# Optimization experiments

Hardware: AMD Instinct MI355X
Metric: run time of the kernel (lower is better)

Reference implementation:

```python
import jax, jax.numpy as jnp
import numpy as np

B, S, H = 1, 4096, 2048
NH, NKV, HD = 16, 4, 128  # query heads, kv heads, head_dim
THETA = 1000000.0
NEG = -1e9


def setup_inputs() -> dict:
    key = jax.random.key(0)
    ks = jax.random.split(key, 5)
    hidden_states = jax.random.normal(ks[0], (B, S, H), jnp.float32) * 0.02
    Wq = jax.random.normal(ks[1], (H, NH * HD), jnp.float32) * 0.02
    Wk = jax.random.normal(ks[2], (H, NKV * HD), jnp.float32) * 0.02
    Wv = jax.random.normal(ks[3], (H, NKV * HD), jnp.float32) * 0.02
    Wo = jax.random.normal(ks[4], (H, H), jnp.float32) * 0.02
    # additive causal mask [B,1,S,S]
    causal = jnp.tril(jnp.ones((S, S), bool))
    attention_mask = jnp.where(causal, 0.0, NEG).astype(jnp.float32)[None, None]
    position_ids = jnp.arange(S, dtype=jnp.int32)[None]
    return dict(hidden_states=hidden_states, Wq=Wq, Wk=Wk, Wv=Wv, Wo=Wo,
                attention_mask=attention_mask, position_ids=position_ids)


def _rotate_half(x):
    return jnp.concatenate([-x[..., HD // 2:], x[..., :HD // 2]], axis=-1)


def reference(hidden_states, Wq, Wk, Wv, Wo, attention_mask, position_ids):
    # projections -> [B, heads, S, HD]
    q = (hidden_states @ Wq).reshape(B, S, NH, HD).transpose(0, 2, 1, 3)
    k = (hidden_states @ Wk).reshape(B, S, NKV, HD).transpose(0, 2, 1, 3)
    v = (hidden_states @ Wv).reshape(B, S, NKV, HD).transpose(0, 2, 1, 3)

    # RoPE (HF style: freqs duplicated across halves, rotate_half)
    inv_freq = 1.0 / (THETA ** (jnp.arange(0, HD, 2, dtype=jnp.float32) / HD))
    freqs = position_ids.astype(jnp.float32)[..., None] * inv_freq  # [B,S,HD/2]
    emb = jnp.concatenate([freqs, freqs], axis=-1)                  # [B,S,HD]
    cos = jnp.cos(emb)[:, None].astype(q.dtype)                     # [B,1,S,HD]
    sin = jnp.sin(emb)[:, None].astype(q.dtype)
    q = q * cos + _rotate_half(q) * sin
    k = k * cos + _rotate_half(k) * sin

    # GQA: repeat each kv head consecutively (matches torch repeat_kv)
    rep = NH // NKV
    k = jnp.repeat(k, rep, axis=1)
    v = jnp.repeat(v, rep, axis=1)

    scale = 1.0 / jnp.sqrt(jnp.float32(HD))
    scores = jnp.einsum('bhqd,bhkd->bhqk', q, k) * scale + attention_mask
    attn = jax.nn.softmax(scores.astype(jnp.float32), axis=-1).astype(q.dtype)
    out = jnp.einsum('bhqk,bhkd->bhqd', attn, v)  # [B,NH,S,HD]
    out = out.transpose(0, 2, 1, 3).reshape(B, S, H)
    return out @ Wo
```

## Files before the change

### kernel.cpp

```cpp
#include <hip/hip_runtime.h>
#include <stdint.h>

typedef uint16_t u16;
typedef __bf16  bf16x8 __attribute__((ext_vector_type(8)));
typedef float   f32x4  __attribute__((ext_vector_type(4)));
typedef float   f32x16 __attribute__((ext_vector_type(16)));
typedef uint16_t u16x8 __attribute__((ext_vector_type(8), may_alias));
typedef uint32_t u32x4 __attribute__((ext_vector_type(4)));

typedef const __attribute__((address_space(1))) void* gas_p;
typedef __attribute__((address_space(3))) void* las_p;

#define SCALE2 0.1275430214486847f

__device__ __forceinline__ void load_lds16(const void* g, void* l) {
    __builtin_amdgcn_global_load_lds((gas_p)g, (las_p)l, 16, 0, 0);
}

__device__ __forceinline__ u16 f2bf(float f) {
    uint32_t u = __builtin_bit_cast(uint32_t, f);
    u += 0x7FFFu + ((u >> 16) & 1u);
    return (u16)(u >> 16);
}
__device__ __forceinline__ float bf2f(u16 h) {
    uint32_t u = ((uint32_t)h) << 16;
    return __builtin_bit_cast(float, u);
}
__device__ __forceinline__ bf16x8 ld_frag(const u16* p) {
    u16x8 t = *(const u16x8*)p;
    return __builtin_bit_cast(bf16x8, t);
}
__device__ __forceinline__ uint32_t cvt_pk_bf16(float lo, float hi) {
    uint32_t r;
    asm("v_cvt_pk_bf16_f32 %0, %1, %2" : "=v"(r) : "v"(lo), "v"(hi));
    return r;
}
__device__ __forceinline__ void plane32_swap(uint32_t& a, uint32_t& b) {
    asm("v_permlane32_swap_b32 %0, %1" : "+v"(a), "+v"(b));
}

__global__ __launch_bounds__(256) void convert_hidden(const float* __restrict__ in,
                                                      u16* __restrict__ out, int n8) {
    int i = blockIdx.x * 256 + threadIdx.x;
    if (i >= n8) return;
    const float* p = in + (size_t)i * 8;
    u16x8 o;
#pragma unroll
    for (int j = 0; j < 8; j++) o[j] = f2bf(p[j]);
    *(u16x8*)(out + (size_t)i * 8) = o;
}

__global__ __launch_bounds__(256) void transpose_cvt(const float* __restrict__ in,
                                                     u16* __restrict__ out,
                                                     int R, int C) {
    __shared__ u16 tile[64][65];
    const int tx = threadIdx.x;
    const int bc = blockIdx.x * 64;
    const int br = blockIdx.y * 64;
#pragma unroll
    for (int i = 0; i < 16; i++) {
        int idx = tx + i * 256;
        int r = idx >> 6, c = idx & 63;
        tile[r][c] = f2bf(in[(size_t)(br + r) * C + bc + c]);
    }
    __syncthreads();
#pragma unroll
    for (int i = 0; i < 16; i++) {
        int idx = tx + i * 256;
        int r = idx >> 6, c = idx & 63;
        out[(size_t)(bc + r) * R + br + c] = tile[c][r];
    }
}

__global__ __launch_bounds__(256) void transpose_b16(const u16* __restrict__ in,
                                                     u16* __restrict__ out,
                                                     int R, int C, int ldin, int off) {
    __shared__ u16 tile[64][65];
    const int tx = threadIdx.x;
    const int bc = blockIdx.x * 64;
    const int br = blockIdx.y * 64;
#pragma unroll
    for (int i = 0; i < 16; i++) {
        int idx = tx + i * 256;
        int r = idx >> 6, c = idx & 63;
        tile[r][c] = in[(size_t)(br + r) * ldin + off + bc + c];
    }
    __syncthreads();
#pragma unroll
    for (int i = 0; i < 16; i++) {
        int idx = tx + i * 256;
        int r = idx >> 6, c = idx & 63;
        out[(size_t)(bc + r) * R + br + c] = tile[c][r];
    }
}

#define TM 128
#define TN 128
#define TK 32

__global__ __launch_bounds__(256) void gemm_qkv(const u16* __restrict__ A,
                                                const u16* __restrict__ WqT,
                                                const u16* __restrict__ WkvT,
                                                u16* __restrict__ Qb,
                                                u16* __restrict__ KVb) {
    __shared__ u16 As[TM * TK];
    __shared__ u16 Bs[TN * TK];
    const int K = 2048;
    const int tid  = threadIdx.x;
    const int wave = tid >> 6;
    const int lane = tid & 63;
    const int l15  = lane & 15;
    const int quad = lane >> 4;
    const int m0 = blockIdx.y * TM;
    const int n0 = blockIdx.x * TN;
    const u16* Bt;
    u16* C;
    int ldC, cbase;
    if (n0 < 2048) { Bt = WqT + (size_t)n0 * K;          C = Qb;  ldC = 2048; cbase = n0; }
    else           { Bt = WkvT + (size_t)(n0 - 2048) * K; C = KVb; ldC = 1024; cbase = n0 - 2048; }
    const int wm = (wave >> 1) * 64;
    const int wn = (wave & 1) * 64;

    f32x4 acc[4][4] = {};

    const int srow = tid >> 2;
    const int scol = (tid & 3) * 8;
    const u16* Ap0 = A  + (size_t)(m0 + srow) * K + scol;
    const u16* Ap1 = A  + (size_t)(m0 + 64 + srow) * K + scol;
    const u16* Bp0 = Bt + (size_t)srow * K + scol;
    const u16* Bp1 = Bt + (size_t)(64 + srow) * K + scol;
    u16* AsD0 = As + wave * 512;
    u16* AsD1 = As + 2048 + wave * 512;
    u16* BsD0 = Bs + wave * 512;
    u16* BsD1 = Bs + 2048 + wave * 512;

    for (int k0 = 0; k0 < K; k0 += TK) {
        load_lds16(Ap0 + k0, AsD0);
        load_lds16(Ap1 + k0, AsD1);
        load_lds16(Bp0 + k0, BsD0);
        load_lds16(Bp1 + k0, BsD1);
        __syncthreads();
        bf16x8 af[4], bfr[4];
#pragma unroll
        for (int i = 0; i < 4; i++)
            af[i] = ld_frag(&As[(wm + i * 16 + l15) * TK + quad * 8]);
#pragma unroll
        for (int j = 0; j < 4; j++)
            bfr[j] = ld_frag(&Bs[(wn + j * 16 + l15) * TK + quad * 8]);
#pragma unroll
        for (int i = 0; i < 4; i++)
#pragma unroll
            for (int j = 0; j < 4; j++)
                acc[i][j] = __builtin_amdgcn_mfma_f32_16x16x32_bf16(af[i], bfr[j], acc[i][j], 0, 0, 0);
        __syncthreads();
    }
#pragma unroll
    for (int i = 0; i < 4; i++)
#pragma unroll
        for (int j = 0; j < 4; j++)
#pragma unroll
            for (int r = 0; r < 4; r++) {
                int row = m0 + wm + i * 16 + quad * 4 + r;
                int col = cbase + wn + j * 16 + l15;
                C[(size_t)row * ldC + col] = f2bf(acc[i][j][r]);
            }
}

template <bool F32OUT>
__global__ __launch_bounds__(256) void gemm_bt(const u16* __restrict__ A,
                                               const u16* __restrict__ Bt,
                                               void* __restrict__ Cp,
                                               int M, int N, int K) {
    __shared__ u16 As[TM * TK];
    __shared__ u16 Bs[TN * TK];
    const int tid  = threadIdx.x;
    const int wave = tid >> 6;
    const int lane = tid & 63;
    const int l15  = lane & 15;
    const int quad = lane >> 4;
    const int m0 = blockIdx.y * TM;
    const int n0 = blockIdx.x * TN;
    const int wm = (wave >> 1) * 64;
    const int wn = (wave & 1) * 64;

    f32x4 acc[4][4] = {};

    const int srow = tid >> 2;
    const int scol = (tid & 3) * 8;
    const u16* Ap0 = A  + (size_t)(m0 + srow) * K + scol;
    const u16* Ap1 = A  + (size_t)(m0 + 64 + srow) * K + scol;
    const u16* Bp0 = Bt + (size_t)(n0 + srow) * K + scol;
    const u16* Bp1 = Bt + (size_t)(n0 + 64 + srow) * K + scol;
    u16* AsD0 = As + wave * 512;
    u16* AsD1 = As + 2048 + wave * 512;
    u16* BsD0 = Bs + wave * 512;
    u16* BsD1 = Bs + 2048 + wave * 512;

    for (int k0 = 0; k0 < K; k0 += TK) {
        load_lds16(Ap0 + k0, AsD0);
        load_lds16(Ap1 + k0, AsD1);
        load_lds16(Bp0 + k0, BsD0);
        load_lds16(Bp1 + k0, BsD1);
        __syncthreads();
        bf16x8 af[4], bfr[4];
#pragma unroll
        for (int i = 0; i < 4; i++)
            af[i] = ld_frag(&As[(wm + i * 16 + l15) * TK + quad * 8]);
#pragma unroll
        for (int j = 0; j < 4; j++)
            bfr[j] = ld_frag(&Bs[(wn + j * 16 + l15) * TK + quad * 8]);
#pragma unroll
        for (int i = 0; i < 4; i++)
#pragma unroll
            for (int j = 0; j < 4; j++)
                acc[i][j] = __builtin_amdgcn_mfma_f32_16x16x32_bf16(af[i], bfr[j], acc[i][j], 0, 0, 0);
        __syncthreads();
    }
#pragma unroll
    for (int i = 0; i < 4; i++)
#pragma unroll
        for (int j = 0; j < 4; j++)
#pragma unroll
            for (int r = 0; r < 4; r++) {
                int row = m0 + wm + i * 16 + quad * 4 + r;
                int col = n0 + wn + j * 16 + l15;
                if (F32OUT)
                    ((float*)Cp)[(size_t)row * N + col] = acc[i][j][r];
                else
                    ((u16*)Cp)[(size_t)row * N + col] = f2bf(acc[i][j][r]);
            }
}

__global__ __launch_bounds__(256) void rope_kernel(u16* __restrict__ Q,
                                                   u16* __restrict__ KV) {
    int g = blockIdx.x * 256 + threadIdx.x;
    int d = g & 63;
    int row = g >> 6;
    int s = row / 20;
    int hh = row - s * 20;
    u16* buf = (hh < 16) ? (Q + (size_t)s * 2048 + hh * 128)
                         : (KV + (size_t)s * 1024 + (hh - 16) * 128);
    float p = (float)s;
    float angle = p * exp2f((float)d * (-19.931568569324174f / 64.0f));
    float sc = (hh < 16) ? SCALE2 : 1.0f;
    float c = cosf(angle) * sc, sn = sinf(angle) * sc;
    float x0 = bf2f(buf[d]), x1 = bf2f(buf[d + 64]);
    buf[d]      = f2bf(x0 * c - x1 * sn);
    buf[d + 64] = f2bf(x1 * c + x0 * sn);
}

#define QK1(CC, MSK)                                                           \
  do {                                                                         \
    const int krow_ = (CC) * 32 + l31;                                         \
    f32x16 sv_ = {};                                                           \
    _Pragma("unroll")                                                          \
    for (int dk = 0; dk < 8; dk++) {                                           \
      bf16x8 kf = ld_frag(&Kb[krow_ * 128 + (((dk * 2 + hi8) + krow_) & 15) * 8]); \
      sv_ = __builtin_amdgcn_mfma_f32_32x32x16_bf16(kf, qf[dk], sv_, 0, 0, 0); \
    }                                                                          \
    float p_[16]; float rs_ = 0.f;                                             \
    const int kvbs_ = kv0 + (CC) * 32 + 4 * hi8;                               \
    _Pragma("unroll")                                                          \
    for (int r = 0; r < 16; r++) {                                             \
      float pe = exp2f(sv_[r]);                                                \
      if (MSK) { int kvv = kvbs_ + (r & 3) + 8 * (r >> 2);                     \
                 pe = (kvv <= qrow) ? pe : 0.f; }                              \
      p_[r] = pe; rs_ += pe;                                                   \
    }                                                                          \
    lr += rs_;                                                                 \
    uint32_t w0 = cvt_pk_bf16(p_[0], p_[1]);                                   \
    uint32_t w1 = cvt_pk_bf16(p_[2], p_[3]);                                   \
    uint32_t w2 = cvt_pk_bf16(p_[4], p_[5]);                                   \
    uint32_t w3 = cvt_pk_bf16(p_[6], p_[7]);                                   \
    plane32_swap(w0, w2); plane32_swap(w1, w3);                                \
    uint32_t w4 = cvt_pk_bf16(p_[8], p_[9]);                                   \
    uint32_t w5 = cvt_pk_bf16(p_[10], p_[11]);                                 \
    uint32_t w6 = cvt_pk_bf16(p_[12], p_[13]);                                 \
    plane32_swap(w4, w6);                                                      \
    uint32_t w7 = cvt_pk_bf16(p_[14], p_[15]);                                 \
    plane32_swap(w5, w7);                                                      \
    u32x4 a0_ = {w0, w1, w2, w3}, a1_ = {w4, w5, w6, w7};                      \
    bf16x8 pa0_ = __builtin_bit_cast(bf16x8, a0_);                             \
    bf16x8 pa1_ = __builtin_bit_cast(bf16x8, a1_);                             \
    _Pragma("unroll")                                                          \
    for (int ks2 = 0; ks2 < 2; ks2++) {                                        \
      bf16x8 pa_ = ks2 ? pa1_ : pa0_;                                          \
      _Pragma("unroll")                                                        \
      for (int nt = 0; nt < 4; nt++) {                                         \
        const int d_ = nt * 32 + l31;                                          \
        bf16x8 vf = ld_frag(&Vb[d_ * 64 + ((((CC) * 4 + ks2 * 2 + hi8) + d_) & 7) * 8]); \
        acc[nt] = __builtin_amdgcn_mfma_f32_32x32x16_bf16(pa_, vf, acc[nt], 0, 0, 0); \
      }                                                                        \
    }                                                                          \
  } while (0)

__global__ __launch_bounds__(256, 2) void flash_attn9(const u16* __restrict__ Q,
                                                      const u16* __restrict__ KVb,
                                                      const u16* __restrict__ VT,
                                                      u16* __restrict__ Op0,
                                                      u16* __restrict__ Op1,
                                                      float* __restrict__ Lp) {
    __shared__ u16 Ks[2][8192];
    __shared__ u16 Vs[2][8192];
    const int tid  = threadIdx.x;
    const int ww   = tid >> 6;
    const int lane = tid & 63;
    const int l31  = lane & 31;
    const int hi8  = lane >> 5;
    const int bid  = blockIdx.x;
    const int h    = (bid & 7) * 2 + ((bid >> 3) & 1);
    const int rest = bid >> 4;
    const int j    = 31 - (rest >> 1);
    const int s    = rest & 1;
    const int kvh  = h >> 2;
    const int qg0  = j * 128 + ww * 32;
    const int qrow = qg0 + l31;
    const int dW   = qg0 >> 6;
    const int kb0  = s * (j + 1);
    const int kb1  = kb0 + (j + 1);

    bf16x8 qf[8];
    {
        const u16* qp = Q + (size_t)qrow * 2048 + h * 128 + hi8 * 8;
#pragma unroll
        for (int dk = 0; dk < 8; dk++) qf[dk] = ld_frag(qp + dk * 16);
    }

    const u16* srcK[4];
    const u16* srcV[4];
#pragma unroll
    for (int r = 0; r < 4; r++) {
        int p = r * 256 + tid;
        int kv = p >> 4;
        srcK[r] = KVb + (size_t)kv * 1024 + kvh * 128 + ((((p & 15) - kv) & 15) * 8);
        int d = p >> 3;
        srcV[r] = VT + (size_t)(kvh * 128 + d) * 4096 + ((((p & 7) - (d & 7)) & 7) * 8);
    }

    f32x16 acc[4] = {};
    float lr = 0.f;

#pragma unroll
    for (int r = 0; r < 4; r++) {
        load_lds16(srcK[r] + (size_t)(kb0 * 64) * 1024, &Ks[0][r * 2048 + ww * 512]);
        load_lds16(srcV[r] + kb0 * 64, &Vs[0][r * 2048 + ww * 512]);
    }
    asm volatile("s_waitcnt vmcnt(0)" ::: "memory");
    __syncthreads();

    for (int kvb = kb0; kvb < kb1; kvb++) {
        const int cur = (kvb - kb0) & 1;
        if (kvb + 1 < kb1) {
            const int kvn = (kvb + 1) * 64;
#pragma unroll
            for (int r = 0; r < 4; r++) {
                load_lds16(srcK[r] + (size_t)kvn * 1024, &Ks[cur ^ 1][r * 2048 + ww * 512]);
                load_lds16(srcV[r] + kvn, &Vs[cur ^ 1][r * 2048 + ww * 512]);
            }
        }
        const u16* Kb = Ks[cur];
        const u16* Vb = Vs[cur];
        const int kv0 = kvb * 64;

        if (kvb < dW) {
            QK1(0, 0);
            QK1(1, 0);
        } else if (kvb == dW) {
            QK1(0, 1);
            QK1(1, 1);
        }

        asm volatile("s_waitcnt vmcnt(0)" ::: "memory");
        __syncthreads();
    }

    float lt = lr + __shfl_xor(lr, 32);
    if (lane < 32) Lp[(s * 16 + h) * 4096 + qg0 + l31] = lt;
    u16* Ops = s ? Op1 : Op0;
#pragma unroll
    for (int r = 0; r < 16; r++) {
        int qr = (r & 3) + 8 * (r >> 2) + 4 * hi8;
        u16* op = Ops + (size_t)(qg0 + qr) * 2048 + h * 128 + l31;
#pragma unroll
        for (int nt = 0; nt < 4; nt++)
            op[nt * 32] = f2bf(acc[nt][r]);
    }
}

__global__ __launch_bounds__(256) void merge_o(u16* __restrict__ o0,
                                               const u16* __restrict__ o1,
                                               const float* __restrict__ Lp) {
    int i = blockIdx.x * 256 + threadIdx.x;
    size_t base = (size_t)i * 8;
    int row = (int)(base >> 11);
    int h   = (int)((base >> 7) & 15);
    float inv = 1.0f / (Lp[h * 4096 + row] + Lp[(16 + h) * 4096 + row]);
    u16x8 a = *(const u16x8*)(o0 + base);
    u16x8 b = *(const u16x8*)(o1 + base);
    u16x8 o;
#pragma unroll
    for (int jj = 0; jj < 8; jj++)
        o[jj] = f2bf((bf2f(a[jj]) + bf2f(b[jj])) * inv);
    *(u16x8*)(o0 + base) = o;
}

__global__ __launch_bounds__(256, 2) void flash_attn7(const u16* __restrict__ Q,
                                                      const u16* __restrict__ KVb,
                                                      const u16* __restrict__ VT,
                                                      u16* __restrict__ O) {
    __shared__ u16 Ks[2][8192];
    __shared__ u16 Vs[2][8192];
    __shared__ float Llds[4][32];
    const int tid  = threadIdx.x;
    const int ww   = tid >> 6;
    const int lane = tid & 63;
    const int l31  = lane & 31;
    const int hi8  = lane >> 5;
    const int bid  = blockIdx.x;
    const int h    = bid >> 5;
    const int cls  = bid & 31;
    const int bx   = cls >> 1;
    const int z    = cls & 1;
    const int kvh  = h >> 2;
    const int qt0  = z ? (3968 - bx * 128) : (bx * 128);
    const int qg0  = qt0 + ww * 32;
    const int qrow = qg0 + l31;
    const int dW   = qg0 >> 6;
    const int nkv  = (qt0 >> 6) + 2;

    bf16x8 qf[8];
    {
        const u16* qp = Q + (size_t)qrow * 2048 + h * 128 + hi8 * 8;
#pragma unroll
        for (int dk = 0; dk < 8; dk++) qf[dk] = ld_frag(qp + dk * 16);
    }

    const u16* srcK[4];
    const u16* srcV[4];
#pragma unroll
    for (int r = 0; r < 4; r++) {
        int p = r * 256 + tid;
        int kv = p >> 4;
        srcK[r] = KVb + (size_t)kv * 1024 + kvh * 128 + ((((p & 15) - kv) & 15) * 8);
        int d = p >> 3;
        srcV[r] = VT + (size_t)(kvh * 128 + d) * 4096 + ((((p & 7) - (d & 7)) & 7) * 8);
    }

    f32x16 acc[4] = {};
    float lr = 0.f;

#pragma unroll
    for (int r = 0; r < 4; r++) {
        load_lds16(srcK[r], &Ks[0][r * 2048 + ww * 512]);
        load_lds16(srcV[r], &Vs[0][r * 2048 + ww * 512]);
    }
    asm volatile("s_waitcnt vmcnt(0)" ::: "memory");
    __syncthreads();

    for (int kvb = 0; kvb < nkv; kvb++) {
        const int cur = kvb & 1;
        if (kvb + 1 < nkv) {
            const int kvn = (kvb + 1) * 64;
#pragma unroll
            for (int r = 0; r < 4; r++) {
                load_lds16(srcK[r] + (size_t)kvn * 1024, &Ks[cur ^ 1][r * 2048 + ww * 512]);
                load_lds16(srcV[r] + kvn, &Vs[cur ^ 1][r * 2048 + ww * 512]);
            }
        }
        const u16* Kb = Ks[cur];
        const u16* Vb = Vs[cur];
        const int kv0 = kvb * 64;

        if (kvb < dW) {
            QK1(0, 0);
            QK1(1, 0);
        } else if (kvb == dW) {
            QK1(0, 1);
            QK1(1, 1);
        }

        asm volatile("s_waitcnt vmcnt(0)" ::: "memory");
        __syncthreads();
    }

    float lt = lr + __shfl_xor(lr, 32);
    if (lane < 32) Llds[ww][l31] = lt;
    __syncthreads();
#pragma unroll
    for (int r = 0; r < 16; r++) {
        int qr = (r & 3) + 8 * (r >> 2) + 4 * hi8;
        float linv = 1.0f / Llds[ww][qr];
        u16* op = O + (size_t)(qg0 + qr) * 2048 + h * 128 + l31;
#pragma unroll
        for (int nt = 0; nt < 4; nt++)
            op[nt * 32] = f2bf(acc[nt][r] * linv);
    }
}

extern "C" void kernel_launch(void* const* d_in, const int* in_sizes, int n_in,
                              void* d_out, int out_size, void* d_ws, size_t ws_size,
                              hipStream_t stream) {
    const float* hidden = (const float*)d_in[0];
    const float* Wq = (const float*)d_in[1];
    const float* Wk = (const float*)d_in[2];
    const float* Wv = (const float*)d_in[3];
    const float* Wo = (const float*)d_in[4];
    float* out = (float*)d_out;

    u16* ws   = (u16*)d_ws;
    u16* Hb   = ws;
    u16* Qb   = Hb   + 8388608;
    u16* KVb  = Qb   + 8388608;
    u16* WqT  = KVb  + 4194304;
    u16* WkvT = WqT  + 4194304;
    u16* VT   = WkvT + 2097152;
    u16* Op1  = VT   + 4194304;
    const size_t WS_SPLIT = (size_t)(31457280 + 8388608) * 2;

    convert_hidden<<<4096, 256, 0, stream>>>(hidden, Hb, 1048576);

    transpose_cvt<<<dim3(32, 32), 256, 0, stream>>>(Wq, WqT, 2048, 2048);
    transpose_cvt<<<dim3(8, 32), 256, 0, stream>>>(Wk, WkvT, 2048, 512);
    transpose_cvt<<<dim3(8, 32), 256, 0, stream>>>(Wv, WkvT + 1048576, 2048, 512);

    gemm_qkv<<<dim3(24, 32), 256, 0, stream>>>(Hb, WqT, WkvT, Qb, KVb);

    u16* WoT = WqT;
    transpose_cvt<<<dim3(32, 32), 256, 0, stream>>>(Wo, WoT, 2048, 2048);

    rope_kernel<<<dim3(20480), 256, 0, stream>>>(Qb, KVb);

    transpose_b16<<<dim3(8, 64), 256, 0, stream>>>(KVb, VT, 4096, 512, 1024, 512);

    u16* Ob = Hb;
    if (ws_size >= WS_SPLIT) {
        float* Lp = (float*)WkvT;
        flash_attn9<<<dim3(1024), 256, 0, stream>>>(Qb, KVb, VT, Ob, Op1, Lp);
        merge_o<<<dim3(4096), 256, 0, stream>>>(Ob, Op1, Lp);
    } else {
        flash_attn7<<<dim3(512), 256, 0, stream>>>(Qb, KVb, VT, Ob);
    }

    gemm_bt<true><<<dim3(16, 32), 256, 0, stream>>>(Ob, WoT, out, 4096, 2048, 2048);
}
```

Measured before the change: 388.0 us.

## Split K and V prefetch around QK and PV phases in flash attention

The attention loop now issues the next tile's K loads first and computes QK^T and softmax probabilities for both 32-column chunks into registers. Only then does it issue the next V loads, and it runs the PV MFMAs after a barrier, using partial vmcnt waits so the V prefetch can stay in flight while the current tile is processed. The V tile in LDS also gets a new swizzled layout that packs two d-rows per 128-element row. The gain depends on the hardware memory counters retiring in issue order, and holding the P fragments across the barrier raises register pressure.

```diff
diff --git a/kernel.cpp b/kernel.cpp
--- a/kernel.cpp
+++ b/kernel.cpp
@@ -248,6 +248,57 @@
     buf[d]      = f2bf(x0 * c - x1 * sn);
     buf[d + 64] = f2bf(x1 * c + x0 * sn);
 }
+
+#define QKSM(CC, MSK, PA)                                                      \
+  do {                                                                         \
+    const int krow_ = (CC) * 32 + l31;                                         \
+    f32x16 sv_ = {};                                                           \
+    _Pragma("unroll")                                                          \
+    for (int dk = 0; dk < 8; dk++) {                                           \
+      bf16x8 kf = ld_frag(&Kb[krow_ * 128 + (((dk * 2 + hi8) + krow_) & 15) * 8]); \
+      sv_ = __builtin_amdgcn_mfma_f32_32x32x16_bf16(kf, qf[dk], sv_, 0, 0, 0); \
+    }                                                                          \
+    float p_[16]; float rs_ = 0.f;                                             \
+    const int kvbs_ = kv0 + (CC) * 32 + 4 * hi8;                               \
+    _Pragma("unroll")                                                          \
+    for (int r = 0; r < 16; r++) {                                             \
+      float pe = exp2f(sv_[r]);                                                \
+      if (MSK) { int kvv = kvbs_ + (r & 3) + 8 * (r >> 2);                     \
+                 pe = (kvv <= qrow) ? pe : 0.f; }                              \
+      p_[r] = pe; rs_ += pe;                                                   \
+    }                                                                          \
+    lr += rs_;                                                                 \
+    uint32_t w0 = cvt_pk_bf16(p_[0], p_[1]);                                   \
+    uint32_t w1 = cvt_pk_bf16(p_[2], p_[3]);                                   \
+    uint32_t w2 = cvt_pk_bf16(p_[4], p_[5]);                                   \
+    uint32_t w3 = cvt_pk_bf16(p_[6], p_[7]);                                   \
+    plane32_swap(w0, w2); plane32_swap(w1, w3);                                \
+    uint32_t w4 = cvt_pk_bf16(p_[8], p_[9]);                                   \
+    uint32_t w5 = cvt_pk_bf16(p_[10], p_[11]);                                 \
+    uint32_t w6 = cvt_pk_bf16(p_[12], p_[13]);                                 \
+    plane32_swap(w4, w6);                                                      \
+    uint32_t w7 = cvt_pk_bf16(p_[14], p_[15]);                                 \
+    plane32_swap(w5, w7);                                                      \
+    u32x4 a0_ = {w0, w1, w2, w3}, a1_ = {w4, w5, w6, w7};                      \
+    PA[0] = __builtin_bit_cast(bf16x8, a0_);                                   \
+    PA[1] = __builtin_bit_cast(bf16x8, a1_);                                   \
+  } while (0)
+
+#define PVX(CC, PA)                                                            \
+  do {                                                                         \
+    _Pragma("unroll")                                                          \
+    for (int ks2 = 0; ks2 < 2; ks2++) {                                        \
+      bf16x8 pa_ = PA[ks2];                                                    \
+      _Pragma("unroll")                                                        \
+      for (int nt = 0; nt < 4; nt++) {                                         \
+        const int d_ = nt * 32 + l31;                                          \
+        const int vr_ = d_ >> 1;                                               \
+        const int s_ = (d_ & 1) * 8 + ((((CC) * 4 + ks2 * 2 + hi8) + vr_) & 7);\
+        bf16x8 vf = ld_frag(&Vb[vr_ * 128 + s_ * 8]);                          \
+        acc[nt] = __builtin_amdgcn_mfma_f32_32x32x16_bf16(pa_, vf, acc[nt], 0, 0, 0); \
+      }                                                                        \
+    }                                                                          \
+  } while (0)
 
 #define QK1(CC, MSK)                                                           \
   do {                                                                         \
@@ -294,12 +345,12 @@
     }                                                                          \
   } while (0)
 
-__global__ __launch_bounds__(256, 2) void flash_attn9(const u16* __restrict__ Q,
-                                                      const u16* __restrict__ KVb,
-                                                      const u16* __restrict__ VT,
-                                                      u16* __restrict__ Op0,
-                                                      u16* __restrict__ Op1,
-                                                      float* __restrict__ Lp) {
+__global__ __launch_bounds__(256, 2) void flash_attn10(const u16* __restrict__ Q,
+                                                       const u16* __restrict__ KVb,
+                                                       const u16* __restrict__ VT,
+                                                       u16* __restrict__ Op0,
+                                                       u16* __restrict__ Op1,
+                                                       float* __restrict__ Lp) {
     __shared__ u16 Ks[2][8192];
     __shared__ u16 Vs[2][8192];
     const int tid  = threadIdx.x;
@@ -333,45 +384,65 @@
         int p = r * 256 + tid;
         int kv = p >> 4;
         srcK[r] = KVb + (size_t)kv * 1024 + kvh * 128 + ((((p & 15) - kv) & 15) * 8);
-        int d = p >> 3;
-        srcV[r] = VT + (size_t)(kvh * 128 + d) * 4096 + ((((p & 7) - (d & 7)) & 7) * 8);
+        int vr = p >> 4;
+        int sl = p & 15;
+        int d  = 2 * vr + (sl >> 3);
+        int wv = ((sl & 7) - (vr & 7)) & 7;
+        srcV[r] = VT + (size_t)(kvh * 128 + d) * 4096 + wv * 8;
     }
 
     f32x16 acc[4] = {};
     float lr = 0.f;
 
 #pragma unroll
-    for (int r = 0; r < 4; r++) {
+    for (int r = 0; r < 4; r++)
         load_lds16(srcK[r] + (size_t)(kb0 * 64) * 1024, &Ks[0][r * 2048 + ww * 512]);
+#pragma unroll
+    for (int r = 0; r < 4; r++)
         load_lds16(srcV[r] + kb0 * 64, &Vs[0][r * 2048 + ww * 512]);
-    }
     asm volatile("s_waitcnt vmcnt(0)" ::: "memory");
     __syncthreads();
 
     for (int kvb = kb0; kvb < kb1; kvb++) {
         const int cur = (kvb - kb0) & 1;
-        if (kvb + 1 < kb1) {
-            const int kvn = (kvb + 1) * 64;
-#pragma unroll
-            for (int r = 0; r < 4; r++) {
+        const bool pre = (kvb + 1 < kb1);
+        const int kvn = (kvb + 1) * 64;
+        if (pre) {
+#pragma unroll
+            for (int r = 0; r < 4; r++)
                 load_lds16(srcK[r] + (size_t)kvn * 1024, &Ks[cur ^ 1][r * 2048 + ww * 512]);
-                load_lds16(srcV[r] + kvn, &Vs[cur ^ 1][r * 2048 + ww * 512]);
-            }
         }
         const u16* Kb = Ks[cur];
         const u16* Vb = Vs[cur];
         const int kv0 = kvb * 64;
-
-        if (kvb < dW) {
-            QK1(0, 0);
-            QK1(1, 0);
-        } else if (kvb == dW) {
-            QK1(0, 1);
-            QK1(1, 1);
+        const bool act = (kvb <= dW);
+        const bool msk = (kvb == dW);
+
+        bf16x8 pa0[2], pa1[2];
+        if (act) {
+            if (msk) { QKSM(0, 1, pa0); QKSM(1, 1, pa1); }
+            else     { QKSM(0, 0, pa0); QKSM(1, 0, pa1); }
         }
 
-        asm volatile("s_waitcnt vmcnt(0)" ::: "memory");
+        if (pre) {
+#pragma unroll
+            for (int r = 0; r < 4; r++)
+                load_lds16(srcV[r] + kvn, &Vs[cur ^ 1][r * 2048 + ww * 512]);
+            asm volatile("s_waitcnt vmcnt(8)" ::: "memory");
+        } else {
+            asm volatile("s_waitcnt vmcnt(0)" ::: "memory");
+        }
         __syncthreads();
+
+        if (act) {
+            PVX(0, pa0);
+            PVX(1, pa1);
+        }
+
+        if (pre) {
+            asm volatile("s_waitcnt vmcnt(4)" ::: "memory");
+            __syncthreads();
+        }
     }
 
     float lt = lr + __shfl_xor(lr, 32);
@@ -535,7 +606,7 @@
     u16* Ob = Hb;
     if (ws_size >= WS_SPLIT) {
         float* Lp = (float*)WkvT;
-        flash_attn9<<<dim3(1024), 256, 0, stream>>>(Qb, KVb, VT, Ob, Op1, Lp);
+        flash_attn10<<<dim3(1024), 256, 0, stream>>>(Qb, KVb, VT, Ob, Op1, Lp);
         merge_o<<<dim3(4096), 256, 0, stream>>>(Ob, Op1, Lp);
     } else {
         flash_attn7<<<dim3(512), 256, 0, stream>>>(Qb, KVb, VT, Ob);
```

New measurement: 393.2 us. Within noise of the previous version (+1.3%).

## Double GEMM K-tile with XOR-swizzled LDS and merge small prep kernels

Applied to the files above, without the earlier changes.

Both bf16 GEMMs (QKV projection and output projection) now stage 64-wide K slices instead of 32. The LDS layout uses an XOR swizzle on 16-byte chunks so fragment reads avoid bank conflicts, and there are half as many barrier pairs per K. The hidden conversion and the three weight transposes are merged into one `prep` launch. RoPE, the Wo transpose and the V transpose are merged into one `mid` launch, which cuts kernel launch and tail overhead. LDS per GEMM block doubles, which may lower occupancy.

```diff
diff --git a/kernel.cpp b/kernel.cpp
--- a/kernel.cpp
+++ b/kernel.cpp
@@ -39,24 +39,32 @@
     asm("v_permlane32_swap_b32 %0, %1" : "+v"(a), "+v"(b));
 }
 
-__global__ __launch_bounds__(256) void convert_hidden(const float* __restrict__ in,
-                                                      u16* __restrict__ out, int n8) {
-    int i = blockIdx.x * 256 + threadIdx.x;
-    if (i >= n8) return;
-    const float* p = in + (size_t)i * 8;
-    u16x8 o;
-#pragma unroll
-    for (int j = 0; j < 8; j++) o[j] = f2bf(p[j]);
-    *(u16x8*)(out + (size_t)i * 8) = o;
-}
-
-__global__ __launch_bounds__(256) void transpose_cvt(const float* __restrict__ in,
-                                                     u16* __restrict__ out,
-                                                     int R, int C) {
+__global__ __launch_bounds__(256) void prep(const float* __restrict__ hidden,
+                                            u16* __restrict__ Hb,
+                                            const float* __restrict__ Wq,
+                                            u16* __restrict__ WqT,
+                                            const float* __restrict__ Wk,
+                                            const float* __restrict__ Wv,
+                                            u16* __restrict__ WkvT) {
     __shared__ u16 tile[64][65];
-    const int tx = threadIdx.x;
-    const int bc = blockIdx.x * 64;
-    const int br = blockIdx.y * 64;
+    const int bid = blockIdx.x;
+    const int tx  = threadIdx.x;
+    if (bid < 4096) {
+        int i = bid * 256 + tx;
+        const float* p = hidden + (size_t)i * 8;
+        u16x8 o;
+#pragma unroll
+        for (int j = 0; j < 8; j++) o[j] = f2bf(p[j]);
+        *(u16x8*)(Hb + (size_t)i * 8) = o;
+        return;
+    }
+    const float* in;
+    u16* out;
+    int R, C, bx, by;
+    if (bid < 5120)      { int l = bid - 4096; in = Wq; out = WqT;            R = 2048; C = 2048; bx = l & 31; by = l >> 5; }
+    else if (bid < 5376) { int l = bid - 5120; in = Wk; out = WkvT;           R = 2048; C = 512;  bx = l & 7;  by = l >> 3; }
+    else                 { int l = bid - 5376; in = Wv; out = WkvT + 1048576; R = 2048; C = 512;  bx = l & 7;  by = l >> 3; }
+    const int bc = bx * 64, br = by * 64;
 #pragma unroll
     for (int i = 0; i < 16; i++) {
         int idx = tx + i * 256;
@@ -72,39 +80,78 @@
     }
 }
 
-__global__ __launch_bounds__(256) void transpose_b16(const u16* __restrict__ in,
-                                                     u16* __restrict__ out,
-                                                     int R, int C, int ldin, int off) {
+__global__ __launch_bounds__(256) void mid(u16* __restrict__ Q,
+                                           u16* __restrict__ KV,
+                                           const float* __restrict__ Wo,
+                                           u16* __restrict__ WoT,
+                                           u16* __restrict__ VT) {
     __shared__ u16 tile[64][65];
-    const int tx = threadIdx.x;
-    const int bc = blockIdx.x * 64;
-    const int br = blockIdx.y * 64;
-#pragma unroll
-    for (int i = 0; i < 16; i++) {
-        int idx = tx + i * 256;
-        int r = idx >> 6, c = idx & 63;
-        tile[r][c] = in[(size_t)(br + r) * ldin + off + bc + c];
-    }
-    __syncthreads();
-#pragma unroll
-    for (int i = 0; i < 16; i++) {
-        int idx = tx + i * 256;
-        int r = idx >> 6, c = idx & 63;
-        out[(size_t)(bc + r) * R + br + c] = tile[c][r];
+    const int bid = blockIdx.x;
+    const int tx  = threadIdx.x;
+    if (bid < 20480) {
+        int g = bid * 256 + tx;
+        int d = g & 63;
+        int row = g >> 6;
+        int s = row / 20;
+        int hh = row - s * 20;
+        u16* buf = (hh < 16) ? (Q + (size_t)s * 2048 + hh * 128)
+                             : (KV + (size_t)s * 1024 + (hh - 16) * 128);
+        float p = (float)s;
+        float angle = p * exp2f((float)d * (-19.931568569324174f / 64.0f));
+        float sc = (hh < 16) ? SCALE2 : 1.0f;
+        float c = cosf(angle) * sc, sn = sinf(angle) * sc;
+        float x0 = bf2f(buf[d]), x1 = bf2f(buf[d + 64]);
+        buf[d]      = f2bf(x0 * c - x1 * sn);
+        buf[d + 64] = f2bf(x1 * c + x0 * sn);
+        return;
+    }
+    if (bid < 21504) {
+        int l = bid - 20480;
+        int bc = (l & 31) * 64, br = (l >> 5) * 64;
+#pragma unroll
+        for (int i = 0; i < 16; i++) {
+            int idx = tx + i * 256;
+            int r = idx >> 6, c = idx & 63;
+            tile[r][c] = f2bf(Wo[(size_t)(br + r) * 2048 + bc + c]);
+        }
+        __syncthreads();
+#pragma unroll
+        for (int i = 0; i < 16; i++) {
+            int idx = tx + i * 256;
+            int r = idx >> 6, c = idx & 63;
+            WoT[(size_t)(bc + r) * 2048 + br + c] = tile[c][r];
+        }
+        return;
+    }
+    {
+        int l = bid - 21504;
+        int bc = (l & 7) * 64, br = (l >> 3) * 64;
+#pragma unroll
+        for (int i = 0; i < 16; i++) {
+            int idx = tx + i * 256;
+            int r = idx >> 6, c = idx & 63;
+            tile[r][c] = KV[(size_t)(br + r) * 1024 + 512 + bc + c];
+        }
+        __syncthreads();
+#pragma unroll
+        for (int i = 0; i < 16; i++) {
+            int idx = tx + i * 256;
+            int r = idx >> 6, c = idx & 63;
+            VT[(size_t)(bc + r) * 4096 + br + c] = tile[c][r];
+        }
     }
 }
 
 #define TM 128
 #define TN 128
-#define TK 32
 
 __global__ __launch_bounds__(256) void gemm_qkv(const u16* __restrict__ A,
                                                 const u16* __restrict__ WqT,
                                                 const u16* __restrict__ WkvT,
                                                 u16* __restrict__ Qb,
                                                 u16* __restrict__ KVb) {
-    __shared__ u16 As[TM * TK];
-    __shared__ u16 Bs[TN * TK];
+    __shared__ u16 As[128 * 64];
+    __shared__ u16 Bs[128 * 64];
     const int K = 2048;
     const int tid  = threadIdx.x;
     const int wave = tid >> 6;
@@ -123,35 +170,40 @@
 
     f32x4 acc[4][4] = {};
 
-    const int srow = tid >> 2;
-    const int scol = (tid & 3) * 8;
-    const u16* Ap0 = A  + (size_t)(m0 + srow) * K + scol;
-    const u16* Ap1 = A  + (size_t)(m0 + 64 + srow) * K + scol;
-    const u16* Bp0 = Bt + (size_t)srow * K + scol;
-    const u16* Bp1 = Bt + (size_t)(64 + srow) * K + scol;
-    u16* AsD0 = As + wave * 512;
-    u16* AsD1 = As + 2048 + wave * 512;
-    u16* BsD0 = Bs + wave * 512;
-    u16* BsD1 = Bs + 2048 + wave * 512;
-
-    for (int k0 = 0; k0 < K; k0 += TK) {
-        load_lds16(Ap0 + k0, AsD0);
-        load_lds16(Ap1 + k0, AsD1);
-        load_lds16(Bp0 + k0, BsD0);
-        load_lds16(Bp1 + k0, BsD1);
-        __syncthreads();
-        bf16x8 af[4], bfr[4];
-#pragma unroll
-        for (int i = 0; i < 4; i++)
-            af[i] = ld_frag(&As[(wm + i * 16 + l15) * TK + quad * 8]);
-#pragma unroll
-        for (int j = 0; j < 4; j++)
-            bfr[j] = ld_frag(&Bs[(wn + j * 16 + l15) * TK + quad * 8]);
-#pragma unroll
-        for (int i = 0; i < 4; i++)
-#pragma unroll
-            for (int j = 0; j < 4; j++)
-                acc[i][j] = __builtin_amdgcn_mfma_f32_16x16x32_bf16(af[i], bfr[j], acc[i][j], 0, 0, 0);
+    const int srow = tid >> 3;
+    const int swc  = ((tid & 7) ^ (srow & 7)) * 8;
+    const u16* Ap[4];
+    const u16* Bp[4];
+#pragma unroll
+    for (int r = 0; r < 4; r++) {
+        Ap[r] = A  + (size_t)(m0 + srow + r * 32) * K + swc;
+        Bp[r] = Bt + (size_t)(srow + r * 32) * K + swc;
+    }
+    u16* AsD = As + wave * 512;
+    u16* BsD = Bs + wave * 512;
+
+    for (int k0 = 0; k0 < K; k0 += 64) {
+#pragma unroll
+        for (int r = 0; r < 4; r++) load_lds16(Ap[r] + k0, AsD + r * 2048);
+#pragma unroll
+        for (int r = 0; r < 4; r++) load_lds16(Bp[r] + k0, BsD + r * 2048);
+        __syncthreads();
+        bf16x8 af[2][4], bfr[2][4];
+        const int sx = (l15 & 7) << 3;
+#pragma unroll
+        for (int kk = 0; kk < 2; kk++)
+#pragma unroll
+            for (int i = 0; i < 4; i++) {
+                af[kk][i]  = ld_frag(&As[((wm + i * 16 + l15) * 64 + kk * 32 + quad * 8) ^ sx]);
+                bfr[kk][i] = ld_frag(&Bs[((wn + i * 16 + l15) * 64 + kk * 32 + quad * 8) ^ sx]);
+            }
+#pragma unroll
+        for (int kk = 0; kk < 2; kk++)
+#pragma unroll
+            for (int i = 0; i < 4; i++)
+#pragma unroll
+                for (int j = 0; j < 4; j++)
+                    acc[i][j] = __builtin_amdgcn_mfma_f32_16x16x32_bf16(af[kk][i], bfr[kk][j], acc[i][j], 0, 0, 0);
         __syncthreads();
     }
 #pragma unroll
@@ -171,8 +223,8 @@
                                                const u16* __restrict__ Bt,
                                                void* __restrict__ Cp,
                                                int M, int N, int K) {
-    __shared__ u16 As[TM * TK];
-    __shared__ u16 Bs[TN * TK];
+    __shared__ u16 As[128 * 64];
+    __shared__ u16 Bs[128 * 64];
     const int tid  = threadIdx.x;
     const int wave = tid >> 6;
     const int lane = tid & 63;
@@ -185,35 +237,40 @@
 
     f32x4 acc[4][4] = {};
 
-    const int srow = tid >> 2;
-    const int scol = (tid & 3) * 8;
-    const u16* Ap0 = A  + (size_t)(m0 + srow) * K + scol;
-    const u16* Ap1 = A  + (size_t)(m0 + 64 + srow) * K + scol;
-    const u16* Bp0 = Bt + (size_t)(n0 + srow) * K + scol;
-    const u16* Bp1 = Bt + (size_t)(n0 + 64 + srow) * K + scol;
-    u16* AsD0 = As + wave * 512;
-    u16* AsD1 = As + 2048 + wave * 512;
-    u16* BsD0 = Bs + wave * 512;
-    u16* BsD1 = Bs + 2048 + wave * 512;
-
-    for (int k0 = 0; k0 < K; k0 += TK) {
-        load_lds16(Ap0 + k0, AsD0);
-        load_lds16(Ap1 + k0, AsD1);
-        load_lds16(Bp0 + k0, BsD0);
-        load_lds16(Bp1 + k0, BsD1);
-        __syncthreads();
-        bf16x8 af[4], bfr[4];
-#pragma unroll
-        for (int i = 0; i < 4; i++)
-            af[i] = ld_frag(&As[(wm + i * 16 + l15) * TK + quad * 8]);
-#pragma unroll
-        for (int j = 0; j < 4; j++)
-            bfr[j] = ld_frag(&Bs[(wn + j * 16 + l15) * TK + quad * 8]);
-#pragma unroll
-        for (int i = 0; i < 4; i++)
-#pragma unroll
-            for (int j = 0; j < 4; j++)
-                acc[i][j] = __builtin_amdgcn_mfma_f32_16x16x32_bf16(af[i], bfr[j], acc[i][j], 0, 0, 0);
+    const int srow = tid >> 3;
+    const int swc  = ((tid & 7) ^ (srow & 7)) * 8;
+    const u16* Ap[4];
+    const u16* Bp[4];
+#pragma unroll
+    for (int r = 0; r < 4; r++) {
+        Ap[r] = A  + (size_t)(m0 + srow + r * 32) * K + swc;
+        Bp[r] = Bt + (size_t)(n0 + srow + r * 32) * K + swc;
+    }
+    u16* AsD = As + wave * 512;
+    u16* BsD = Bs + wave * 512;
+
+    for (int k0 = 0; k0 < K; k0 += 64) {
+#pragma unroll
+        for (int r = 0; r < 4; r++) load_lds16(Ap[r] + k0, AsD + r * 2048);
+#pragma unroll
+        for (int r = 0; r < 4; r++) load_lds16(Bp[r] + k0, BsD + r * 2048);
+        __syncthreads();
+        bf16x8 af[2][4], bfr[2][4];
+        const int sx = (l15 & 7) << 3;
+#pragma unroll
+        for (int kk = 0; kk < 2; kk++)
+#pragma unroll
+            for (int i = 0; i < 4; i++) {
+                af[kk][i]  = ld_frag(&As[((wm + i * 16 + l15) * 64 + kk * 32 + quad * 8) ^ sx]);
+                bfr[kk][i] = ld_frag(&Bs[((wn + i * 16 + l15) * 64 + kk * 32 + quad * 8) ^ sx]);
+            }
+#pragma unroll
+        for (int kk = 0; kk < 2; kk++)
+#pragma unroll
+            for (int i = 0; i < 4; i++)
+#pragma unroll
+                for (int j = 0; j < 4; j++)
+                    acc[i][j] = __builtin_amdgcn_mfma_f32_16x16x32_bf16(af[kk][i], bfr[kk][j], acc[i][j], 0, 0, 0);
         __syncthreads();
     }
 #pragma unroll
@@ -229,24 +286,6 @@
                 else
                     ((u16*)Cp)[(size_t)row * N + col] = f2bf(acc[i][j][r]);
             }
-}
-
-__global__ __launch_bounds__(256) void rope_kernel(u16* __restrict__ Q,
-                                                   u16* __restrict__ KV) {
-    int g = blockIdx.x * 256 + threadIdx.x;
-    int d = g & 63;
-    int row = g >> 6;
-    int s = row / 20;
-    int hh = row - s * 20;
-    u16* buf = (hh < 16) ? (Q + (size_t)s * 2048 + hh * 128)
-                         : (KV + (size_t)s * 1024 + (hh - 16) * 128);
-    float p = (float)s;
-    float angle = p * exp2f((float)d * (-19.931568569324174f / 64.0f));
-    float sc = (hh < 16) ? SCALE2 : 1.0f;
-    float c = cosf(angle) * sc, sn = sinf(angle) * sc;
-    float x0 = bf2f(buf[d]), x1 = bf2f(buf[d + 64]);
-    buf[d]      = f2bf(x0 * c - x1 * sn);
-    buf[d + 64] = f2bf(x1 * c + x0 * sn);
 }
 
 #define QK1(CC, MSK)                                                           \
@@ -517,20 +556,12 @@
     u16* Op1  = VT   + 4194304;
     const size_t WS_SPLIT = (size_t)(31457280 + 8388608) * 2;
 
-    convert_hidden<<<4096, 256, 0, stream>>>(hidden, Hb, 1048576);
-
-    transpose_cvt<<<dim3(32, 32), 256, 0, stream>>>(Wq, WqT, 2048, 2048);
-    transpose_cvt<<<dim3(8, 32), 256, 0, stream>>>(Wk, WkvT, 2048, 512);
-    transpose_cvt<<<dim3(8, 32), 256, 0, stream>>>(Wv, WkvT + 1048576, 2048, 512);
+    prep<<<dim3(5632), 256, 0, stream>>>(hidden, Hb, Wq, WqT, Wk, Wv, WkvT);
 
     gemm_qkv<<<dim3(24, 32), 256, 0, stream>>>(Hb, WqT, WkvT, Qb, KVb);
 
     u16* WoT = WqT;
-    transpose_cvt<<<dim3(32, 32), 256, 0, stream>>>(Wo, WoT, 2048, 2048);
-
-    rope_kernel<<<dim3(20480), 256, 0, stream>>>(Qb, KVb);
-
-    transpose_b16<<<dim3(8, 64), 256, 0, stream>>>(KVb, VT, 4096, 512, 1024, 512);
+    mid<<<dim3(22016), 256, 0, stream>>>(Qb, KVb, Wo, WoT, VT);
 
     u16* Ob = Hb;
     if (ws_size >= WS_SPLIT) {
```

Result: faster. 379.5 us (-2.2%).
